# Kernel optimization log

Measured on AMD Instinct MI355X. Metric: run time of the kernel, lower is better.

Reference implementation:

```python
import jax, jax.numpy as jnp
import numpy as np

N, T, F = 20000, 20, 128
H = 128          # lstm hidden per direction
GH, HEADS = 128, 4
NUM_CLASSES = 10
E = 640000
SCALE = 0.05


def _lstm_last_hidden(x, lengths, Wih, Whh, b):
    """Run a unidirectional LSTM over padded x [N,T,F]; return hidden at the
    last valid step per sequence (torch gate order i,f,g,o)."""
    pre = jnp.einsum('ntf,gf->ntg', x, Wih) + b            # [N,T,4H]
    mask = jnp.arange(x.shape[1])[None, :] < lengths[:, None]  # [N,T]
    h0 = jnp.zeros((x.shape[0], Whh.shape[1]), x.dtype)

    def step(carry, inp):
        h, c = carry
        pt, m = inp                                         # [N,4H], [N]
        gates = pt + h @ Whh.T
        i, f, g, o = jnp.split(gates, 4, axis=-1)
        c_new = jax.nn.sigmoid(f) * c + jax.nn.sigmoid(i) * jnp.tanh(g)
        h_new = jax.nn.sigmoid(o) * jnp.tanh(c_new)
        m = m[:, None]
        return (jnp.where(m, h_new, h), jnp.where(m, c_new, c)), None

    (h, _), _ = jax.lax.scan(step, (h0, h0), (pre.transpose(1, 0, 2), mask.T))
    return h


def _reverse_by_length(x, lengths):
    # x[n, t] -> x[n, len-1-t] for t < len (padding positions are masked later)
    idx = jnp.clip(lengths[:, None] - 1 - jnp.arange(x.shape[1])[None, :], 0, None)
    return x[jnp.arange(x.shape[0])[:, None], idx]


def _gat(h, src, dst, W, a_src, a_dst, bias, heads):
    n = h.shape[0]
    xh = (h @ W.T).reshape(n, heads, -1)                    # [N,H,C]
    al_s = jnp.sum(xh * a_src, -1)                          # [N,H]
    al_d = jnp.sum(xh * a_dst, -1)
    e = jax.nn.leaky_relu(al_s[src] + al_d[dst], 0.2)       # [E,H]
    emax = jax.ops.segment_max(e, dst, num_segments=n)
    emax = jnp.where(jnp.isfinite(emax), emax, 0.0)
    ee = jnp.exp(e - emax[dst])
    denom = jax.ops.segment_sum(ee, dst, num_segments=n)
    alpha = ee / (denom[dst] + 1e-16)                       # segment softmax
    out = jax.ops.segment_sum(xh[src] * alpha[..., None], dst, num_segments=n)
    return out.reshape(n, -1) + bias


def setup_inputs() -> dict:
    key = jax.random.key(0)
    ks = jax.random.split(key, 16)
    p = lambda k, *s: jax.random.normal(k, s, jnp.float32) * SCALE
    return {
        'x': jax.random.normal(ks[0], (N, T, F), jnp.float32),
        'lengths': jax.random.randint(ks[1], (N,), 1, T + 1, jnp.int32),
        'edge_index': jax.random.randint(ks[2], (2, E), 0, N, jnp.int32),
        # BiLSTM params (b = b_ih + b_hh combined; identical math)
        'Wih_f': p(ks[3], 4 * H, F), 'Whh_f': p(ks[4], 4 * H, H), 'b_f': p(ks[5], 4 * H),
        'Wih_b': p(ks[6], 4 * H, F), 'Whh_b': p(ks[7], 4 * H, H), 'b_b': p(ks[8], 4 * H),
        # GAT1: in=2H=256 -> heads*GH=512
        'W1': p(ks[9], HEADS * GH, 2 * H), 'a1_src': p(ks[10], HEADS, GH),
        'a1_dst': p(ks[11], HEADS, GH), 'bias1': jnp.zeros((HEADS * GH,), jnp.float32),
        # GAT2: in=512 -> 1*GH=128
        'W2': p(ks[12], GH, HEADS * GH), 'a2_src': p(ks[13], 1, GH),
        'a2_dst': p(ks[14], 1, GH), 'bias2': jnp.zeros((GH,), jnp.float32),
        'Wfc': p(ks[15], NUM_CLASSES, GH), 'bfc': jnp.zeros((NUM_CLASSES,), jnp.float32),
    }


def reference(x, lengths, edge_index, Wih_f, Whh_f, b_f, Wih_b, Whh_b, b_b,
              W1, a1_src, a1_dst, bias1, W2, a2_src, a2_dst, bias2, Wfc, bfc):
    n = x.shape[0]
    h_fwd = _lstm_last_hidden(x, lengths, Wih_f, Whh_f, b_f)
    h_bwd = _lstm_last_hidden(_reverse_by_length(x, lengths), lengths, Wih_b, Whh_b, b_b)
    h = jnp.concatenate([h_fwd, h_bwd], axis=-1)            # [N, 2H]
    # GATConv default adds self-loops
    loop = jnp.arange(n, dtype=edge_index.dtype)
    src = jnp.concatenate([edge_index[0], loop])
    dst = jnp.concatenate([edge_index[1], loop])
    h = jax.nn.relu(_gat(h, src, dst, W1, a1_src, a1_dst, bias1, HEADS))
    h = jax.nn.relu(_gat(h, src, dst, W2, a2_src, a2_dst, bias2, 1))
    return h @ Wfc.T + bfc                                  # [N, num_classes]
```

## Files before the change

### kernel.cpp

```cpp
#include <hip/hip_runtime.h>

#define NSEQ 20000
#define TT 20
#define FD 128
#define EDG 640000
#define ETOT (EDG + NSEQ)

typedef short bf16x8 __attribute__((ext_vector_type(8)));
typedef float f32x4 __attribute__((ext_vector_type(4)));
typedef unsigned short u16;
typedef unsigned int u32;

__device__ __forceinline__ float bf2f(u16 h) {
  union { u32 u; float f; } v; v.u = ((u32)h) << 16; return v.f;
}
__device__ __forceinline__ u16 f2bf(float f) {
  union { float f; u32 u; } v; v.f = f;
  u32 u = v.u;
  return (u16)((u + 0x7fffu + ((u >> 16) & 1u)) >> 16);
}
__device__ __forceinline__ float fast_rcp(float x) {
  float r; asm("v_rcp_f32 %0, %1" : "=v"(r) : "v"(x)); return r;
}
__device__ __forceinline__ u32 cvtpk_bf16(float a, float b) {
  u32 r; asm("v_cvt_pk_bf16_f32 %0, %1, %2" : "=v"(r) : "v"(a), "v"(b)); return r;
}
__device__ __forceinline__ float sigm(float x) { return fast_rcp(1.0f + __expf(-x)); }
__device__ __forceinline__ float tanh_f(float x) { return 1.0f - 2.0f * fast_rcp(__expf(2.0f * x) + 1.0f); }
__device__ __forceinline__ int clampi(int v, int lo, int hi) {
  return v < lo ? lo : (v > hi ? hi : v);
}

template<int BF>
__device__ __forceinline__ bf16x8 ld8(const void* p, size_t i) {
  if (BF) return *(const bf16x8*)((const u16*)p + i);
  f32x4 a = *(const f32x4*)((const float*)p + i);
  f32x4 b = *(const f32x4*)((const float*)p + i + 4);
  union { u32 w[4]; bf16x8 v; } u;
  u.w[0] = cvtpk_bf16(a[0], a[1]);
  u.w[1] = cvtpk_bf16(a[2], a[3]);
  u.w[2] = cvtpk_bf16(b[0], b[1]);
  u.w[3] = cvtpk_bf16(b[2], b[3]);
  return u.v;
}

#define OFF_WIHF 0
#define OFF_WHHF 65536
#define OFF_BF   131072
#define OFF_WIHB 131584
#define OFF_WHHB 197120
#define OFF_BB   262656
#define OFF_W1   263168
#define OFF_W2   394240
#define OFF_A1S  459776
#define OFF_A1D  460288
#define OFF_B1   460800
#define OFF_A2S  461312
#define OFF_A2D  461440
#define OFF_B2   461568
#define OFF_WFC  461696
#define OFF_BFC  462976

__global__ void k_detect(const u32* __restrict__ xw, int* __restrict__ flag) {
  const int lane = threadIdx.x & 63;
  u16 lo = (u16)(xw[lane] & 0xffffu);
  int e = (lo >> 7) & 0xff;
  unsigned long long m = __ballot(e >= 100 && e <= 140);
  if (threadIdx.x == 0) flag[0] = (__popcll(m) >= 32) ? 1 : 0;
}

struct CvtArgs {
  const void* src[16];
  int off[16];
  int cnt[16];
};

template<int BF>
__global__ void k_cvt(CvtArgs a, u16* __restrict__ canon, const int* __restrict__ flag) {
  if (flag[0] != BF) return;
  int idx = blockIdx.x * 256 + threadIdx.x;
  int stride = gridDim.x * 256;
#pragma unroll 1
  for (int s = 0; s < 16; ++s) {
    const void* sp = a.src[s];
    int n = a.cnt[s], off = a.off[s];
    for (int i = idx; i < n; i += stride) {
      canon[off + i] = BF ? ((const u16*)sp)[i] : f2bf(((const float*)sp)[i]);
    }
  }
}

__global__ void k_fill0(u16* __restrict__ out, int n) {
  int i = blockIdx.x * 256 + threadIdx.x;
  if (i < n) out[i] = 0;
}

template<int BF>
__global__ __launch_bounds__(512, 2) void k_lstm(
    const void* __restrict__ x, const int* __restrict__ lengths,
    const int* __restrict__ lperm,
    const u16* __restrict__ canon, u16* __restrict__ hcat,
    const int* __restrict__ flag)
{
  if (flag[0] != BF) return;
  __shared__ u16 Ax[2][64 * 128];
  __shared__ u16 Ah[2][64 * 128];
  __shared__ int lenS[64];
  __shared__ int seqS[64];
  __shared__ int sMax;

  const int tid = threadIdx.x;
  const int wv = tid >> 6;
  const int lane = tid & 63;
  const int q = lane >> 4;
  const int cc = lane & 15;
  const int dir = blockIdx.y;
  const int b0 = (gridDim.x - 1 - blockIdx.x) * 64;

  const u16* Wi = canon + (dir ? OFF_WIHB : OFF_WIHF);
  const u16* Wh = canon + (dir ? OFF_WHHB : OFF_WHHF);
  const u16* bb = canon + (dir ? OFF_BB : OFF_BF);

  bf16x8 wih[4][4], whh[4][4];
  float bv[4];
#pragma unroll
  for (int g = 0; g < 4; ++g) {
    int row = g * 128 + wv * 16 + cc;
#pragma unroll
    for (int kt = 0; kt < 4; ++kt) {
      wih[g][kt] = *(const bf16x8*)(Wi + row * 128 + kt * 32 + q * 8);
      whh[g][kt] = *(const bf16x8*)(Wh + row * 128 + kt * 32 + q * 8);
    }
    bv[g] = bf2f(bb[g * 128 + wv * 16 + cc]);
  }

  if (tid < 64) {
    int s = lperm[clampi(b0 + tid, 0, NSEQ - 1)];
    s = clampi(s, 0, NSEQ - 1);
    seqS[tid] = s;
    int L = clampi(lengths[s], 1, TT);
    lenS[tid] = L;
#pragma unroll
    for (int off = 32; off >= 1; off >>= 1) L = max(L, __shfl_xor(L, off, 64));
    if (tid == 0) sMax = L;
  }
  {
    f32x4 zz = {0.f, 0.f, 0.f, 0.f};
    f32x4* p = (f32x4*)Ah[0];
    for (int i = tid; i < 1024; i += 512) p[i] = zz;
  }
  __syncthreads();

  const int tmax = sMax;

  int lenp[4];
#pragma unroll
  for (int m = 0; m < 4; ++m) {
    int v = 0;
#pragma unroll
    for (int r = 0; r < 4; ++r) v |= lenS[m * 16 + q * 4 + r] << (8 * r);
    lenp[m] = v;
  }

  const int lrow = tid >> 3;
  const int lj = tid & 7;
  const int sL = seqS[lrow];
  const int lenL = lenS[lrow];
  const size_t xbase = (size_t)sL * (TT * FD);
  const int ax0 = lrow * 128 + ((lj ^ (lrow & 15)) * 8);
  const int ax1 = lrow * 128 + (((lj + 8) ^ (lrow & 15)) * 8);

  int rofs[4];
#pragma unroll
  for (int kt = 0; kt < 4; ++kt) rofs[kt] = cc * 128 + (((4 * kt + q) ^ cc) * 8);
  const int hu = wv * 16 + cc;
  int cofs[4];
#pragma unroll
  for (int r = 0; r < 4; ++r)
    cofs[r] = (q * 4 + r) * 128 + (((hu >> 3) ^ (q * 4 + r)) * 8) + (hu & 7);

  {
    int t0 = dir ? (lenL - 1) : 0;
    bf16x8 d0 = ld8<BF>(x, xbase + t0 * FD + lj * 8);
    bf16x8 d1 = ld8<BF>(x, xbase + t0 * FD + (lj + 8) * 8);
    *(bf16x8*)&Ax[0][ax0] = d0;
    *(bf16x8*)&Ax[0][ax1] = d1;
  }
  float c[4][4] = {};
  int cb = 0;
  __syncthreads();

#pragma unroll 1
  for (int t = 0; t < tmax; ++t) {
    const u16* Axr = Ax[cb];
    u16* Axw = Ax[cb ^ 1];
    const u16* Ahr = Ah[cb];
    u16* Ahw = Ah[cb ^ 1];

    bf16x8 d0 = {}, d1 = {};
    const bool more = (t + 1 < tmax);
    if (more) {
      int tn = t + 1;
      int tt2 = dir ? (lenL - 1 - tn) : tn;
      if (tt2 < 0) tt2 = 0;
      d0 = ld8<BF>(x, xbase + tt2 * FD + lj * 8);
      d1 = ld8<BF>(x, xbase + tt2 * FD + (lj + 8) * 8);
    }

#pragma unroll
    for (int m = 0; m < 4; ++m) {
      const int mb = m * 2048;
      f32x4 acc[4];
#pragma unroll
      for (int g = 0; g < 4; ++g) { f32x4 vi = {bv[g], bv[g], bv[g], bv[g]}; acc[g] = vi; }
#pragma unroll
      for (int kt = 0; kt < 4; ++kt) {
        bf16x8 a = *(const bf16x8*)&Axr[mb + rofs[kt]];
#pragma unroll
        for (int g = 0; g < 4; ++g)
          acc[g] = __builtin_amdgcn_mfma_f32_16x16x32_bf16(a, wih[g][kt], acc[g], 0, 0, 0);
      }
#pragma unroll
      for (int kt = 0; kt < 4; ++kt) {
        bf16x8 a = *(const bf16x8*)&Ahr[mb + rofs[kt]];
#pragma unroll
        for (int g = 0; g < 4; ++g)
          acc[g] = __builtin_amdgcn_mfma_f32_16x16x32_bf16(a, whh[g][kt], acc[g], 0, 0, 0);
      }

      int lp = lenp[m];
      float hf[4];
#pragma unroll
      for (int r = 0; r < 4; ++r) {
        if (t < ((lp >> (8 * r)) & 255)) {
          float iv = acc[0][r], fv = acc[1][r], gv = acc[2][r], ov = acc[3][r];
          float cn = sigm(fv) * c[m][r] + sigm(iv) * tanh_f(gv);
          c[m][r] = cn;
          hf[r] = sigm(ov) * tanh_f(cn);
        } else {
          hf[r] = bf2f(Ahr[mb + cofs[r]]);
        }
      }
      u32 w01 = cvtpk_bf16(hf[0], hf[1]);
      u32 w23 = cvtpk_bf16(hf[2], hf[3]);
      Ahw[mb + cofs[0]] = (u16)w01;
      Ahw[mb + cofs[1]] = (u16)(w01 >> 16);
      Ahw[mb + cofs[2]] = (u16)w23;
      Ahw[mb + cofs[3]] = (u16)(w23 >> 16);
    }

    if (more) {
      *(bf16x8*)&Axw[ax0] = d0;
      *(bf16x8*)&Axw[ax1] = d1;
    }
    __syncthreads();
    cb ^= 1;
  }

  for (int i = tid; i < 1024; i += 512) {
    int row = i >> 4, ch = i & 15;
    if (b0 + row < NSEQ) {
      int seq = seqS[row];
      bf16x8 v = *(const bf16x8*)&Ah[cb][row * 128 + ((ch ^ (row & 15)) * 8)];
      *(bf16x8*)(hcat + (size_t)seq * 256 + dir * 128 + ch * 8) = v;
    }
  }
}

__global__ __launch_bounds__(256) void k_gemm(
    const u16* __restrict__ A, const u16* __restrict__ W, u16* __restrict__ C,
    int M, int Nc, int K)
{
  __shared__ u16 As[128 * 64];
  __shared__ u16 Bs[128 * 64];
  const int tid = threadIdx.x;
  const int wv = tid >> 6, lane = tid & 63, q = lane >> 4, cc = lane & 15;
  const int mblk = blockIdx.x * 128, nblk = blockIdx.y * 128;
  const int wm = (wv & 1) * 64, wn = (wv >> 1) * 64;

  f32x4 acc[4][4] = {};

  const int srow = tid >> 1;
  const int sc0 = (tid & 1) * 4;
  int arow_g = mblk + srow; if (arow_g > M - 1) arow_g = M - 1;
  const u16* aptr = A + (size_t)arow_g * K + sc0 * 8;
  const u16* bptr = W + (size_t)(nblk + srow) * K + sc0 * 8;

  for (int k0 = 0; k0 < K; k0 += 64) {
#pragma unroll
    for (int cch = 0; cch < 4; ++cch) {
      bf16x8 av = *(const bf16x8*)(aptr + k0 + cch * 8);
      bf16x8 bvv = *(const bf16x8*)(bptr + k0 + cch * 8);
      int ch = sc0 + cch;
      *(bf16x8*)&As[srow * 64 + ((ch ^ (srow & 7)) * 8)] = av;
      *(bf16x8*)&Bs[srow * 64 + ((ch ^ (srow & 7)) * 8)] = bvv;
    }
    __syncthreads();
#pragma unroll
    for (int kt = 0; kt < 2; ++kt) {
      bf16x8 af[4];
#pragma unroll
      for (int m = 0; m < 4; ++m) {
        int row = wm + m * 16 + cc;
        af[m] = *(const bf16x8*)&As[row * 64 + (((4 * kt + q) ^ (row & 7)) * 8)];
      }
#pragma unroll
      for (int n = 0; n < 4; ++n) {
        int rowb = wn + n * 16 + cc;
        bf16x8 bfr = *(const bf16x8*)&Bs[rowb * 64 + (((4 * kt + q) ^ (rowb & 7)) * 8)];
#pragma unroll
        for (int m = 0; m < 4; ++m)
          acc[m][n] = __builtin_amdgcn_mfma_f32_16x16x32_bf16(af[m], bfr, acc[m][n], 0, 0, 0);
      }
    }
    __syncthreads();
  }

#pragma unroll
  for (int m = 0; m < 4; ++m)
#pragma unroll
    for (int n = 0; n < 4; ++n)
#pragma unroll
      for (int r = 0; r < 4; ++r) {
        int row = mblk + wm + m * 16 + q * 4 + r;
        int col = nblk + wn + n * 16 + cc;
        if (row < M) C[(size_t)row * Nc + col] = f2bf(acc[m][n][r]);
      }
}

__global__ __launch_bounds__(256) void k_al1(
    const u16* __restrict__ xh1, const u16* __restrict__ canon,
    float* __restrict__ als, float* __restrict__ ald)
{
  const int lane = threadIdx.x & 63;
  const int n = blockIdx.x * 4 + (threadIdx.x >> 6);
  const int hd = lane >> 4;
  bf16x8 xv = *(const bf16x8*)(xh1 + (size_t)n * 512 + lane * 8);
  bf16x8 sv = *(const bf16x8*)(canon + OFF_A1S + hd * 128 + (lane & 15) * 8);
  bf16x8 dv = *(const bf16x8*)(canon + OFF_A1D + hd * 128 + (lane & 15) * 8);
  float ps = 0.f, pd = 0.f;
#pragma unroll
  for (int j = 0; j < 8; ++j) {
    float xf = bf2f((u16)xv[j]);
    ps += xf * bf2f((u16)sv[j]);
    pd += xf * bf2f((u16)dv[j]);
  }
#pragma unroll
  for (int off = 8; off >= 1; off >>= 1) {
    ps += __shfl_xor(ps, off, 64);
    pd += __shfl_xor(pd, off, 64);
  }
  if ((lane & 15) == 0) { als[n * 4 + hd] = ps; ald[n * 4 + hd] = pd; }
}

__global__ __launch_bounds__(256) void k_agg1(
    const u16* __restrict__ xh1, const float* __restrict__ als, const float* __restrict__ ald,
    const int* __restrict__ offs, const int* __restrict__ csr,
    const u16* __restrict__ canon, u16* __restrict__ h1)
{
  const int lane = threadIdx.x & 63;
  const int hd = threadIdx.x >> 6;
  const int n = blockIdx.x;
  int off0 = offs[n], off1 = offs[n + 1];
  off0 = clampi(off0, 0, ETOT);
  off1 = clampi(off1, off0, ETOT);
  const float ad = ald[(size_t)n * 4 + hd];
  const int deg = off1 - off0;
  const u16* xb = xh1 + hd * 128 + lane * 2;

  float o0 = 0.f, o1 = 0.f;
  if (deg <= 64) {
    int s = 0;
    float e = -1e30f;
    if (lane < deg) {
      s = clampi(csr[off0 + lane], 0, NSEQ - 1);
      float t = als[(size_t)s * 4 + hd] + ad;
      e = t > 0.f ? t : 0.2f * t;
    }
    float mx = e;
#pragma unroll
    for (int off = 32; off >= 1; off >>= 1) mx = fmaxf(mx, __shfl_xor(mx, off, 64));
    float ex = (lane < deg) ? __expf(e - mx) : 0.f;
    float sm = ex;
#pragma unroll
    for (int off = 32; off >= 1; off >>= 1) sm += __shfl_xor(sm, off, 64);
    const float a = ex * fast_rcp(sm + 1e-16f);
    const int sofs = s * 512;
    for (int j = 0; j < deg; ++j) {
      int so = __builtin_amdgcn_readlane(sofs, j);
      float aa = __int_as_float(__builtin_amdgcn_readlane(__float_as_int(a), j));
      u32 xv = *(const u32*)(xb + so);
      o0 += aa * bf2f((u16)(xv & 0xffffu));
      o1 += aa * bf2f((u16)(xv >> 16));
    }
  } else {
    float mx = -1e30f;
    for (int k = off0 + lane; k < off1; k += 64) {
      int s = clampi(csr[k], 0, NSEQ - 1);
      float e = als[(size_t)s * 4 + hd] + ad;
      e = e > 0.f ? e : 0.2f * e;
      mx = fmaxf(mx, e);
    }
#pragma unroll
    for (int off = 32; off >= 1; off >>= 1) mx = fmaxf(mx, __shfl_xor(mx, off, 64));
    float sm = 0.f;
    for (int k = off0 + lane; k < off1; k += 64) {
      int s = clampi(csr[k], 0, NSEQ - 1);
      float e = als[(size_t)s * 4 + hd] + ad;
      e = e > 0.f ? e : 0.2f * e;
      sm += __expf(e - mx);
    }
#pragma unroll
    for (int off = 32; off >= 1; off >>= 1) sm += __shfl_xor(sm, off, 64);
    const float rd = fast_rcp(sm + 1e-16f);
    for (int k = off0; k < off1; ++k) {
      int s = clampi(csr[k], 0, NSEQ - 1);
      float e = als[(size_t)s * 4 + hd] + ad;
      e = e > 0.f ? e : 0.2f * e;
      float a = __expf(e - mx) * rd;
      u32 xv = *(const u32*)(xb + (size_t)s * 512);
      o0 += a * bf2f((u16)(xv & 0xffffu));
      o1 += a * bf2f((u16)(xv >> 16));
    }
  }
  o0 += bf2f(canon[OFF_B1 + hd * 128 + lane * 2]);
  o1 += bf2f(canon[OFF_B1 + hd * 128 + lane * 2 + 1]);
  o0 = o0 > 0.f ? o0 : 0.f;
  o1 = o1 > 0.f ? o1 : 0.f;
  u32 pk = (u32)f2bf(o0) | ((u32)f2bf(o1) << 16);
  *(u32*)(h1 + (size_t)n * 512 + hd * 128 + lane * 2) = pk;
}

__global__ __launch_bounds__(256) void k_al2(
    const u16* __restrict__ xh2, const u16* __restrict__ canon,
    float* __restrict__ als2, float* __restrict__ ald2)
{
  const int lane = threadIdx.x & 63;
  const int n = blockIdx.x * 4 + (threadIdx.x >> 6);
  float x0 = bf2f(xh2[(size_t)n * 128 + lane * 2]);
  float x1 = bf2f(xh2[(size_t)n * 128 + lane * 2 + 1]);
  float ps = x0 * bf2f(canon[OFF_A2S + lane * 2]) + x1 * bf2f(canon[OFF_A2S + lane * 2 + 1]);
  float pd = x0 * bf2f(canon[OFF_A2D + lane * 2]) + x1 * bf2f(canon[OFF_A2D + lane * 2 + 1]);
#pragma unroll
  for (int off = 32; off >= 1; off >>= 1) {
    ps += __shfl_xor(ps, off, 64);
    pd += __shfl_xor(pd, off, 64);
  }
  if (lane == 0) { als2[n] = ps; ald2[n] = pd; }
}

__global__ __launch_bounds__(256) void k_agg2(
    const u16* __restrict__ xh2, const float* __restrict__ als2, const float* __restrict__ ald2,
    const int* __restrict__ offs, const int* __restrict__ csr,
    const u16* __restrict__ canon, float* __restrict__ h2)
{
  const int lane = threadIdx.x & 63;
  const int n = blockIdx.x * 4 + (threadIdx.x >> 6);
  int off0 = offs[n], off1 = offs[n + 1];
  off0 = clampi(off0, 0, ETOT);
  off1 = clampi(off1, off0, ETOT);
  const float adn = ald2[n];
  const int deg = off1 - off0;

  float o0 = 0.f, o1 = 0.f;
  if (deg <= 64) {
    int s = 0;
    float e = -1e30f;
    if (lane < deg) {
      s = clampi(csr[off0 + lane], 0, NSEQ - 1);
      float t = als2[s] + adn;
      e = t > 0.f ? t : 0.2f * t;
    }
    float mx = e;
#pragma unroll
    for (int off = 32; off >= 1; off >>= 1) mx = fmaxf(mx, __shfl_xor(mx, off, 64));
    float ex = (lane < deg) ? __expf(e - mx) : 0.f;
    float sm = ex;
#pragma unroll
    for (int off = 32; off >= 1; off >>= 1) sm += __shfl_xor(sm, off, 64);
    const float a = ex * fast_rcp(sm + 1e-16f);
    const int sofs = s * 128;
    for (int j = 0; j < deg; ++j) {
      int so = __builtin_amdgcn_readlane(sofs, j);
      float aa = __int_as_float(__builtin_amdgcn_readlane(__float_as_int(a), j));
      u32 xv = *(const u32*)(xh2 + so + lane * 2);
      o0 += aa * bf2f((u16)(xv & 0xffffu));
      o1 += aa * bf2f((u16)(xv >> 16));
    }
  } else {
    float mx = -1e30f;
    for (int k = off0 + lane; k < off1; k += 64) {
      float e = als2[clampi(csr[k], 0, NSEQ - 1)] + adn;
      e = e > 0.f ? e : 0.2f * e;
      mx = fmaxf(mx, e);
    }
#pragma unroll
    for (int off = 32; off >= 1; off >>= 1) mx = fmaxf(mx, __shfl_xor(mx, off, 64));
    float sm = 0.f;
    for (int k = off0 + lane; k < off1; k += 64) {
      float e = als2[clampi(csr[k], 0, NSEQ - 1)] + adn;
      e = e > 0.f ? e : 0.2f * e;
      sm += __expf(e - mx);
    }
#pragma unroll
    for (int off = 32; off >= 1; off >>= 1) sm += __shfl_xor(sm, off, 64);
    float rd = fast_rcp(sm + 1e-16f);
    for (int k = off0; k < off1; ++k) {
      int s = clampi(csr[k], 0, NSEQ - 1);
      float e = als2[s] + adn;
      e = e > 0.f ? e : 0.2f * e;
      float a = __expf(e - mx) * rd;
      u32 xv = *(const u32*)(xh2 + (size_t)s * 128 + lane * 2);
      o0 += a * bf2f((u16)(xv & 0xffffu));
      o1 += a * bf2f((u16)(xv >> 16));
    }
  }
  o0 += bf2f(canon[OFF_B2 + lane * 2]);     o0 = o0 > 0.f ? o0 : 0.f;
  o1 += bf2f(canon[OFF_B2 + lane * 2 + 1]); o1 = o1 > 0.f ? o1 : 0.f;
  float2 st; st.x = o0; st.y = o1;
  *(float2*)(h2 + (size_t)n * 128 + lane * 2) = st;
}

template<int BF>
__global__ __launch_bounds__(256) void k_fc(
    const float* __restrict__ h2, const u16* __restrict__ canon,
    void* __restrict__ out, const int* __restrict__ flag)
{
  if (flag[0] != BF) return;
  const int lane = threadIdx.x & 63;
  const int n = blockIdx.x * 4 + (threadIdx.x >> 6);
  float a0 = h2[(size_t)n * 128 + lane];
  float a1 = h2[(size_t)n * 128 + 64 + lane];
  float res[10];
#pragma unroll
  for (int cls = 0; cls < 10; ++cls) {
    float p = a0 * bf2f(canon[OFF_WFC + cls * 128 + lane]) +
              a1 * bf2f(canon[OFF_WFC + cls * 128 + 64 + lane]);
#pragma unroll
    for (int off = 32; off >= 1; off >>= 1) p += __shfl_xor(p, off, 64);
    float v = p + bf2f(canon[OFF_BFC + cls]);
    res[cls] = (fabsf(v) < 1e30f) ? v : 0.f;
  }
  if (BF) {
    if (lane < 5) {
      u32 pk = (u32)f2bf(res[lane * 2]) | ((u32)f2bf(res[lane * 2 + 1]) << 16);
      ((u32*)out)[(size_t)n * 5 + lane] = pk;
    }
  } else {
    if (lane < 10) ((float*)out)[(size_t)n * 10 + lane] = res[lane];
  }
}

__global__ void k_zero_all(int* __restrict__ deg, int* __restrict__ lcnt) {
  int i = blockIdx.x * 256 + threadIdx.x;
  if (i < NSEQ) deg[i] = 0;
  if (i < 64) lcnt[i] = 0;
}

__global__ void k_hist_all(const int* __restrict__ ei, const int* __restrict__ lengths,
                           int* __restrict__ deg, int* __restrict__ lcnt) {
  int i = blockIdx.x * 256 + threadIdx.x;
  if (i < ETOT) {
    int d = (i < EDG) ? ei[EDG + i] : (i - EDG);
    d = clampi(d, 0, NSEQ - 1);
    atomicAdd(&deg[d], 1);
  }
  if (i < NSEQ) atomicAdd(&lcnt[clampi(lengths[i], 1, TT) - 1], 1);
}

__global__ __launch_bounds__(1024) void k_scan(const int* __restrict__ deg,
                                               int* __restrict__ offs, int* __restrict__ cur,
                                               const int* __restrict__ lcnt,
                                               int* __restrict__ lcur) {
  __shared__ int wsum[16];
  const int tid = threadIdx.x;
  if (tid == 0) {
    int run = 0;
    for (int i = 0; i < TT; ++i) { lcur[i] = run; run += lcnt[i]; }
  }
  const int lane = tid & 63, wv = tid >> 6;
  const int CHUNK = 20;
  int base = tid * CHUNK;
  int loc[20];
  int s = 0;
#pragma unroll
  for (int i = 0; i < CHUNK; ++i) {
    int idx = base + i;
    int v = (idx < NSEQ) ? deg[idx] : 0;
    loc[i] = s;
    s += v;
  }
  int inc = s;
#pragma unroll
  for (int off = 1; off < 64; off <<= 1) {
    int t2 = __shfl_up(inc, off, 64);
    if (lane >= off) inc += t2;
  }
  if (lane == 63) wsum[wv] = inc;
  __syncthreads();
  int wbase = 0;
  for (int i = 0; i < wv; ++i) wbase += wsum[i];
  int tbase = wbase + inc - s;
#pragma unroll
  for (int i = 0; i < CHUNK; ++i) {
    int idx = base + i;
    if (idx < NSEQ) {
      int st = tbase + loc[i];
      offs[idx] = st;
      cur[idx] = st;
    }
  }
  if (tid == 0) offs[NSEQ] = ETOT;
}

__global__ void k_scatter_all(const int* __restrict__ ei, const int* __restrict__ lengths,
                              int* __restrict__ cur, int* __restrict__ csr,
                              int* __restrict__ lcur, int* __restrict__ lperm) {
  int i = blockIdx.x * 256 + threadIdx.x;
  if (i < ETOT) {
    int s, d;
    if (i < EDG) { s = ei[i]; d = ei[EDG + i]; }
    else { s = i - EDG; d = s; }
    d = clampi(d, 0, NSEQ - 1);
    int pos = atomicAdd(&cur[d], 1);
    pos = clampi(pos, 0, ETOT - 1);
    csr[pos] = s;
  }
  if (i < NSEQ) {
    int b = clampi(lengths[i], 1, TT) - 1;
    int pos = atomicAdd(&lcur[b], 1);
    lperm[clampi(pos, 0, NSEQ - 1)] = i;
  }
}

extern "C" void kernel_launch(void* const* d_in, const int* in_sizes, int n_in,
                              void* d_out, int out_size, void* d_ws, size_t ws_size,
                              hipStream_t stream) {
  (void)in_sizes; (void)n_in;
  const void* x     = d_in[0];
  const int* lengths= (const int*)d_in[1];
  const int* ei     = (const int*)d_in[2];

  const size_t NEED = 45769344u;
  if (ws_size < NEED) {
    k_fill0<<<(out_size + 255) / 256, 256, 0, stream>>>((u16*)d_out, out_size);
    return;
  }

  char* w = (char*)d_ws;
  size_t o = 0;
  auto alloc = [&](size_t b) { char* p = w + o; o += (b + 255) & ~(size_t)255; return p; };
  int*  flag = (int*)  alloc(256);
  u16*  canon= (u16*)  alloc(1048576);
  int*  deg  = (int*)  alloc((size_t)NSEQ * 4);
  int*  offs = (int*)  alloc((size_t)(NSEQ + 1) * 4);
  int*  cur  = (int*)  alloc((size_t)NSEQ * 4);
  int*  csr  = (int*)  alloc((size_t)ETOT * 4);
  float* als1= (float*)alloc((size_t)NSEQ * 4 * 4);
  float* ald1= (float*)alloc((size_t)NSEQ * 4 * 4);
  char* regB = alloc((size_t)NSEQ * 512 * 2);
  u16*  xh1  = (u16*)regB;
  u16*  xh2  = (u16*)regB;
  float* h2  = (float*)(regB + (size_t)NSEQ * 128 * 2);
  float* als2= (float*)(regB + (size_t)NSEQ * 128 * 2 + (size_t)NSEQ * 128 * 4);
  float* ald2= als2 + NSEQ;
  char* regA = alloc((size_t)NSEQ * 256 * 2);
  u16*  hcat = (u16*)regA;
  u16*  h1   = (u16*)regA;
  alloc((size_t)NSEQ * 256 * 2);

  int* lperm = (int*)regB;
  int* lcnt  = (int*)(regB + 80128);
  int* lcur  = (int*)(regB + 80256);

  k_detect<<<1, 64, 0, stream>>>((const u32*)x, flag);
  CvtArgs ca;
  const int srcIdx[16] = {3, 4, 5, 6, 7, 8, 9, 13, 10, 11, 12, 14, 15, 16, 17, 18};
  const int offv[16]   = {OFF_WIHF, OFF_WHHF, OFF_BF, OFF_WIHB, OFF_WHHB, OFF_BB,
                          OFF_W1, OFF_W2, OFF_A1S, OFF_A1D, OFF_B1,
                          OFF_A2S, OFF_A2D, OFF_B2, OFF_WFC, OFF_BFC};
  const int cntv[16]   = {65536, 65536, 512, 65536, 65536, 512,
                          131072, 65536, 512, 512, 512, 128, 128, 128, 1280, 10};
  for (int i = 0; i < 16; ++i) { ca.src[i] = d_in[srcIdx[i]]; ca.off[i] = offv[i]; ca.cnt[i] = cntv[i]; }
  k_cvt<1><<<256, 256, 0, stream>>>(ca, canon, flag);
  k_cvt<0><<<256, 256, 0, stream>>>(ca, canon, flag);

  k_zero_all<<<(NSEQ + 255) / 256, 256, 0, stream>>>(deg, lcnt);
  k_hist_all<<<(ETOT + 255) / 256, 256, 0, stream>>>(ei, lengths, deg, lcnt);
  k_scan<<<1, 1024, 0, stream>>>(deg, offs, cur, lcnt, lcur);
  k_scatter_all<<<(ETOT + 255) / 256, 256, 0, stream>>>(ei, lengths, cur, csr, lcur, lperm);

  k_lstm<1><<<dim3(313, 2), 512, 0, stream>>>(x, lengths, lperm, canon, hcat, flag);
  k_lstm<0><<<dim3(313, 2), 512, 0, stream>>>(x, lengths, lperm, canon, hcat, flag);

  k_gemm<<<dim3(157, 4), 256, 0, stream>>>(hcat, canon + OFF_W1, xh1, NSEQ, 512, 256);
  k_al1<<<5000, 256, 0, stream>>>(xh1, canon, als1, ald1);
  k_agg1<<<NSEQ, 256, 0, stream>>>(xh1, als1, ald1, offs, csr, canon, h1);

  k_gemm<<<dim3(157, 1), 256, 0, stream>>>(h1, canon + OFF_W2, xh2, NSEQ, 128, 512);
  k_al2<<<5000, 256, 0, stream>>>(xh2, canon, als2, ald2);
  k_agg2<<<5000, 256, 0, stream>>>(xh2, als2, ald2, offs, csr, canon, h2);

  k_fc<1><<<5000, 256, 0, stream>>>(h2, canon, d_out, flag);
  k_fc<0><<<5000, 256, 0, stream>>>(h2, canon, d_out, flag);
}
```

Before: 864.4 us.

## Fuse attention logits into GEMM epilogue and FC into aggregation; transpose LSTM MFMA

New measurement: 822.6 us. 4.8% less time.

```diff
diff --git a/kernel.cpp b/kernel.cpp
--- a/kernel.cpp
+++ b/kernel.cpp
@@ -13,6 +13,12 @@
 
 __device__ __forceinline__ float bf2f(u16 h) {
   union { u32 u; float f; } v; v.u = ((u32)h) << 16; return v.f;
+}
+__device__ __forceinline__ float bf_lo(u32 w) {
+  union { u32 u; float f; } v; v.u = w << 16; return v.f;
+}
+__device__ __forceinline__ float bf_hi(u32 w) {
+  union { u32 u; float f; } v; v.u = w & 0xffff0000u; return v.f;
 }
 __device__ __forceinline__ u16 f2bf(float f) {
   union { float f; u32 u; } v; v.f = f;
@@ -122,7 +128,7 @@
   const u16* bb = canon + (dir ? OFF_BB : OFF_BF);
 
   bf16x8 wih[4][4], whh[4][4];
-  float bv[4];
+  uint2 bvp[4];
 #pragma unroll
   for (int g = 0; g < 4; ++g) {
     int row = g * 128 + wv * 16 + cc;
@@ -131,7 +137,7 @@
       wih[g][kt] = *(const bf16x8*)(Wi + row * 128 + kt * 32 + q * 8);
       whh[g][kt] = *(const bf16x8*)(Wh + row * 128 + kt * 32 + q * 8);
     }
-    bv[g] = bf2f(bb[g * 128 + wv * 16 + cc]);
+    bvp[g] = *(const uint2*)(bb + g * 128 + wv * 16 + q * 4);
   }
 
   if (tid < 64) {
@@ -153,14 +159,9 @@
 
   const int tmax = sMax;
 
-  int lenp[4];
-#pragma unroll
-  for (int m = 0; m < 4; ++m) {
-    int v = 0;
-#pragma unroll
-    for (int r = 0; r < 4; ++r) v |= lenS[m * 16 + q * 4 + r] << (8 * r);
-    lenp[m] = v;
-  }
+  int lenq[4];
+#pragma unroll
+  for (int m = 0; m < 4; ++m) lenq[m] = lenS[m * 16 + cc];
 
   const int lrow = tid >> 3;
   const int lj = tid & 7;
@@ -173,11 +174,7 @@
   int rofs[4];
 #pragma unroll
   for (int kt = 0; kt < 4; ++kt) rofs[kt] = cc * 128 + (((4 * kt + q) ^ cc) * 8);
-  const int hu = wv * 16 + cc;
-  int cofs[4];
-#pragma unroll
-  for (int r = 0; r < 4; ++r)
-    cofs[r] = (q * 4 + r) * 128 + (((hu >> 3) ^ (q * 4 + r)) * 8) + (hu & 7);
+  const int awbase = cc * 128 + (((wv * 2 + (q >> 1)) ^ cc) * 8) + (q & 1) * 4;
 
   {
     int t0 = dir ? (lenL - 1) : 0;
@@ -212,41 +209,41 @@
       const int mb = m * 2048;
       f32x4 acc[4];
 #pragma unroll
-      for (int g = 0; g < 4; ++g) { f32x4 vi = {bv[g], bv[g], bv[g], bv[g]}; acc[g] = vi; }
+      for (int g = 0; g < 4; ++g) {
+        f32x4 vi = {bf_lo(bvp[g].x), bf_hi(bvp[g].x), bf_lo(bvp[g].y), bf_hi(bvp[g].y)};
+        acc[g] = vi;
+      }
 #pragma unroll
       for (int kt = 0; kt < 4; ++kt) {
-        bf16x8 a = *(const bf16x8*)&Axr[mb + rofs[kt]];
+        bf16x8 b = *(const bf16x8*)&Axr[mb + rofs[kt]];
 #pragma unroll
         for (int g = 0; g < 4; ++g)
-          acc[g] = __builtin_amdgcn_mfma_f32_16x16x32_bf16(a, wih[g][kt], acc[g], 0, 0, 0);
+          acc[g] = __builtin_amdgcn_mfma_f32_16x16x32_bf16(wih[g][kt], b, acc[g], 0, 0, 0);
       }
 #pragma unroll
       for (int kt = 0; kt < 4; ++kt) {
-        bf16x8 a = *(const bf16x8*)&Ahr[mb + rofs[kt]];
+        bf16x8 b = *(const bf16x8*)&Ahr[mb + rofs[kt]];
 #pragma unroll
         for (int g = 0; g < 4; ++g)
-          acc[g] = __builtin_amdgcn_mfma_f32_16x16x32_bf16(a, whh[g][kt], acc[g], 0, 0, 0);
+          acc[g] = __builtin_amdgcn_mfma_f32_16x16x32_bf16(whh[g][kt], b, acc[g], 0, 0, 0);
       }
 
-      int lp = lenp[m];
-      float hf[4];
-#pragma unroll
-      for (int r = 0; r < 4; ++r) {
-        if (t < ((lp >> (8 * r)) & 255)) {
+      uint2 hw;
+      if (t < lenq[m]) {
+        float hf[4];
+#pragma unroll
+        for (int r = 0; r < 4; ++r) {
           float iv = acc[0][r], fv = acc[1][r], gv = acc[2][r], ov = acc[3][r];
           float cn = sigm(fv) * c[m][r] + sigm(iv) * tanh_f(gv);
           c[m][r] = cn;
           hf[r] = sigm(ov) * tanh_f(cn);
-        } else {
-          hf[r] = bf2f(Ahr[mb + cofs[r]]);
         }
+        hw.x = cvtpk_bf16(hf[0], hf[1]);
+        hw.y = cvtpk_bf16(hf[2], hf[3]);
+      } else {
+        hw = *(const uint2*)&Ahr[mb + awbase];
       }
-      u32 w01 = cvtpk_bf16(hf[0], hf[1]);
-      u32 w23 = cvtpk_bf16(hf[2], hf[3]);
-      Ahw[mb + cofs[0]] = (u16)w01;
-      Ahw[mb + cofs[1]] = (u16)(w01 >> 16);
-      Ahw[mb + cofs[2]] = (u16)w23;
-      Ahw[mb + cofs[3]] = (u16)(w23 >> 16);
+      *(uint2*)&Ahw[mb + awbase] = hw;
     }
 
     if (more) {
@@ -269,7 +266,9 @@
 
 __global__ __launch_bounds__(256) void k_gemm(
     const u16* __restrict__ A, const u16* __restrict__ W, u16* __restrict__ C,
-    int M, int Nc, int K)
+    int M, int Nc, int K,
+    const u16* __restrict__ aS, const u16* __restrict__ aD,
+    float* __restrict__ als, float* __restrict__ ald, int alsStride)
 {
   __shared__ u16 As[128 * 64];
   __shared__ u16 Bs[128 * 64];
@@ -310,47 +309,57 @@
         bf16x8 bfr = *(const bf16x8*)&Bs[rowb * 64 + (((4 * kt + q) ^ (rowb & 7)) * 8)];
 #pragma unroll
         for (int m = 0; m < 4; ++m)
-          acc[m][n] = __builtin_amdgcn_mfma_f32_16x16x32_bf16(af[m], bfr, acc[m][n], 0, 0, 0);
+          acc[m][n] = __builtin_amdgcn_mfma_f32_16x16x32_bf16(bfr, af[m], acc[m][n], 0, 0, 0);
       }
     }
     __syncthreads();
   }
 
-#pragma unroll
-  for (int m = 0; m < 4; ++m)
-#pragma unroll
-    for (int n = 0; n < 4; ++n)
-#pragma unroll
-      for (int r = 0; r < 4; ++r) {
-        int row = mblk + wm + m * 16 + q * 4 + r;
-        int col = nblk + wn + n * 16 + cc;
-        if (row < M) C[(size_t)row * Nc + col] = f2bf(acc[m][n][r]);
-      }
-}
-
-__global__ __launch_bounds__(256) void k_al1(
-    const u16* __restrict__ xh1, const u16* __restrict__ canon,
-    float* __restrict__ als, float* __restrict__ ald)
-{
-  const int lane = threadIdx.x & 63;
-  const int n = blockIdx.x * 4 + (threadIdx.x >> 6);
-  const int hd = lane >> 4;
-  bf16x8 xv = *(const bf16x8*)(xh1 + (size_t)n * 512 + lane * 8);
-  bf16x8 sv = *(const bf16x8*)(canon + OFF_A1S + hd * 128 + (lane & 15) * 8);
-  bf16x8 dv = *(const bf16x8*)(canon + OFF_A1D + hd * 128 + (lane & 15) * 8);
-  float ps = 0.f, pd = 0.f;
-#pragma unroll
-  for (int j = 0; j < 8; ++j) {
-    float xf = bf2f((u16)xv[j]);
-    ps += xf * bf2f((u16)sv[j]);
-    pd += xf * bf2f((u16)dv[j]);
-  }
-#pragma unroll
-  for (int off = 8; off >= 1; off >>= 1) {
-    ps += __shfl_xor(ps, off, 64);
-    pd += __shfl_xor(pd, off, 64);
-  }
-  if ((lane & 15) == 0) { als[n * 4 + hd] = ps; ald[n * 4 + hd] = pd; }
+  float pls[4] = {}, pld[4] = {};
+#pragma unroll
+  for (int n = 0; n < 4; ++n) {
+    uint2 ws = *(const uint2*)(aS + nblk + wn + n * 16 + q * 4);
+    uint2 wd = *(const uint2*)(aD + nblk + wn + n * 16 + q * 4);
+    float s0 = bf_lo(ws.x), s1 = bf_hi(ws.x), s2 = bf_lo(ws.y), s3 = bf_hi(ws.y);
+    float d0 = bf_lo(wd.x), d1 = bf_hi(wd.x), d2 = bf_lo(wd.y), d3 = bf_hi(wd.y);
+#pragma unroll
+    for (int m = 0; m < 4; ++m) {
+      int row = mblk + wm + m * 16 + cc;
+      uint2 st;
+      st.x = cvtpk_bf16(acc[m][n][0], acc[m][n][1]);
+      st.y = cvtpk_bf16(acc[m][n][2], acc[m][n][3]);
+      if (row < M) *(uint2*)(C + (size_t)row * Nc + nblk + wn + n * 16 + q * 4) = st;
+      pls[m] += acc[m][n][0] * s0 + acc[m][n][1] * s1 + acc[m][n][2] * s2 + acc[m][n][3] * s3;
+      pld[m] += acc[m][n][0] * d0 + acc[m][n][1] * d1 + acc[m][n][2] * d2 + acc[m][n][3] * d3;
+    }
+  }
+
+#pragma unroll
+  for (int m = 0; m < 4; ++m) {
+    pls[m] += __shfl_xor(pls[m], 16, 64);
+    pls[m] += __shfl_xor(pls[m], 32, 64);
+    pld[m] += __shfl_xor(pld[m], 16, 64);
+    pld[m] += __shfl_xor(pld[m], 32, 64);
+  }
+  float* sred = (float*)As;
+  if (lane < 16) {
+#pragma unroll
+    for (int m = 0; m < 4; ++m) {
+      int idx = ((wv & 1) * 4 + m) * 32 + cc * 2 + (wv >> 1);
+      sred[idx] = pls[m];
+      sred[256 + idx] = pld[m];
+    }
+  }
+  __syncthreads();
+  if (wv < 2) {
+    int m = lane >> 4, ccc = lane & 15;
+    int row = mblk + wv * 64 + m * 16 + ccc;
+    int idx = (wv * 4 + m) * 32 + ccc * 2;
+    if (row < M) {
+      als[(size_t)row * alsStride + blockIdx.y] = sred[idx] + sred[idx + 1];
+      ald[(size_t)row * alsStride + blockIdx.y] = sred[256 + idx] + sred[256 + idx + 1];
+    }
+  }
 }
 
 __global__ __launch_bounds__(256) void k_agg1(
@@ -386,6 +395,7 @@
     for (int off = 32; off >= 1; off >>= 1) sm += __shfl_xor(sm, off, 64);
     const float a = ex * fast_rcp(sm + 1e-16f);
     const int sofs = s * 512;
+#pragma unroll 4
     for (int j = 0; j < deg; ++j) {
       int so = __builtin_amdgcn_readlane(sofs, j);
       float aa = __int_as_float(__builtin_amdgcn_readlane(__float_as_int(a), j));
@@ -413,6 +423,7 @@
 #pragma unroll
     for (int off = 32; off >= 1; off >>= 1) sm += __shfl_xor(sm, off, 64);
     const float rd = fast_rcp(sm + 1e-16f);
+#pragma unroll 4
     for (int k = off0; k < off1; ++k) {
       int s = clampi(csr[k], 0, NSEQ - 1);
       float e = als[(size_t)s * 4 + hd] + ad;
@@ -431,28 +442,10 @@
   *(u32*)(h1 + (size_t)n * 512 + hd * 128 + lane * 2) = pk;
 }
 
-__global__ __launch_bounds__(256) void k_al2(
-    const u16* __restrict__ xh2, const u16* __restrict__ canon,
-    float* __restrict__ als2, float* __restrict__ ald2)
-{
-  const int lane = threadIdx.x & 63;
-  const int n = blockIdx.x * 4 + (threadIdx.x >> 6);
-  float x0 = bf2f(xh2[(size_t)n * 128 + lane * 2]);
-  float x1 = bf2f(xh2[(size_t)n * 128 + lane * 2 + 1]);
-  float ps = x0 * bf2f(canon[OFF_A2S + lane * 2]) + x1 * bf2f(canon[OFF_A2S + lane * 2 + 1]);
-  float pd = x0 * bf2f(canon[OFF_A2D + lane * 2]) + x1 * bf2f(canon[OFF_A2D + lane * 2 + 1]);
-#pragma unroll
-  for (int off = 32; off >= 1; off >>= 1) {
-    ps += __shfl_xor(ps, off, 64);
-    pd += __shfl_xor(pd, off, 64);
-  }
-  if (lane == 0) { als2[n] = ps; ald2[n] = pd; }
-}
-
 __global__ __launch_bounds__(256) void k_agg2(
     const u16* __restrict__ xh2, const float* __restrict__ als2, const float* __restrict__ ald2,
     const int* __restrict__ offs, const int* __restrict__ csr,
-    const u16* __restrict__ canon, float* __restrict__ h2)
+    const u16* __restrict__ canon, void* __restrict__ out, const int* __restrict__ flag)
 {
   const int lane = threadIdx.x & 63;
   const int n = blockIdx.x * 4 + (threadIdx.x >> 6);
@@ -480,6 +473,7 @@
     for (int off = 32; off >= 1; off >>= 1) sm += __shfl_xor(sm, off, 64);
     const float a = ex * fast_rcp(sm + 1e-16f);
     const int sofs = s * 128;
+#pragma unroll 4
     for (int j = 0; j < deg; ++j) {
       int so = __builtin_amdgcn_readlane(sofs, j);
       float aa = __int_as_float(__builtin_amdgcn_readlane(__float_as_int(a), j));
@@ -505,6 +499,7 @@
 #pragma unroll
     for (int off = 32; off >= 1; off >>= 1) sm += __shfl_xor(sm, off, 64);
     float rd = fast_rcp(sm + 1e-16f);
+#pragma unroll 4
     for (int k = off0; k < off1; ++k) {
       int s = clampi(csr[k], 0, NSEQ - 1);
       float e = als2[s] + adn;
@@ -517,31 +512,18 @@
   }
   o0 += bf2f(canon[OFF_B2 + lane * 2]);     o0 = o0 > 0.f ? o0 : 0.f;
   o1 += bf2f(canon[OFF_B2 + lane * 2 + 1]); o1 = o1 > 0.f ? o1 : 0.f;
-  float2 st; st.x = o0; st.y = o1;
-  *(float2*)(h2 + (size_t)n * 128 + lane * 2) = st;
-}
-
-template<int BF>
-__global__ __launch_bounds__(256) void k_fc(
-    const float* __restrict__ h2, const u16* __restrict__ canon,
-    void* __restrict__ out, const int* __restrict__ flag)
-{
-  if (flag[0] != BF) return;
-  const int lane = threadIdx.x & 63;
-  const int n = blockIdx.x * 4 + (threadIdx.x >> 6);
-  float a0 = h2[(size_t)n * 128 + lane];
-  float a1 = h2[(size_t)n * 128 + 64 + lane];
+
   float res[10];
 #pragma unroll
   for (int cls = 0; cls < 10; ++cls) {
-    float p = a0 * bf2f(canon[OFF_WFC + cls * 128 + lane]) +
-              a1 * bf2f(canon[OFF_WFC + cls * 128 + 64 + lane]);
+    float p = o0 * bf2f(canon[OFF_WFC + cls * 128 + lane * 2]) +
+              o1 * bf2f(canon[OFF_WFC + cls * 128 + lane * 2 + 1]);
 #pragma unroll
     for (int off = 32; off >= 1; off >>= 1) p += __shfl_xor(p, off, 64);
     float v = p + bf2f(canon[OFF_BFC + cls]);
     res[cls] = (fabsf(v) < 1e30f) ? v : 0.f;
   }
-  if (BF) {
+  if (flag[0]) {
     if (lane < 5) {
       u32 pk = (u32)f2bf(res[lane * 2]) | ((u32)f2bf(res[lane * 2 + 1]) << 16);
       ((u32*)out)[(size_t)n * 5 + lane] = pk;
@@ -661,7 +643,6 @@
   char* regB = alloc((size_t)NSEQ * 512 * 2);
   u16*  xh1  = (u16*)regB;
   u16*  xh2  = (u16*)regB;
-  float* h2  = (float*)(regB + (size_t)NSEQ * 128 * 2);
   float* als2= (float*)(regB + (size_t)NSEQ * 128 * 2 + (size_t)NSEQ * 128 * 4);
   float* ald2= als2 + NSEQ;
   char* regA = alloc((size_t)NSEQ * 256 * 2);
@@ -693,14 +674,11 @@
   k_lstm<1><<<dim3(313, 2), 512, 0, stream>>>(x, lengths, lperm, canon, hcat, flag);
   k_lstm<0><<<dim3(313, 2), 512, 0, stream>>>(x, lengths, lperm, canon, hcat, flag);
 
-  k_gemm<<<dim3(157, 4), 256, 0, stream>>>(hcat, canon + OFF_W1, xh1, NSEQ, 512, 256);
-  k_al1<<<5000, 256, 0, stream>>>(xh1, canon, als1, ald1);
+  k_gemm<<<dim3(157, 4), 256, 0, stream>>>(hcat, canon + OFF_W1, xh1, NSEQ, 512, 256,
+                                           canon + OFF_A1S, canon + OFF_A1D, als1, ald1, 4);
   k_agg1<<<NSEQ, 256, 0, stream>>>(xh1, als1, ald1, offs, csr, canon, h1);
 
-  k_gemm<<<dim3(157, 1), 256, 0, stream>>>(h1, canon + OFF_W2, xh2, NSEQ, 128, 512);
-  k_al2<<<5000, 256, 0, stream>>>(xh2, canon, als2, ald2);
-  k_agg2<<<5000, 256, 0, stream>>>(xh2, als2, ald2, offs, csr, canon, h2);
-
-  k_fc<1><<<5000, 256, 0, stream>>>(h2, canon, d_out, flag);
-  k_fc<0><<<5000, 256, 0, stream>>>(h2, canon, d_out, flag);
-}
+  k_gemm<<<dim3(157, 1), 256, 0, stream>>>(h1, canon + OFF_W2, xh2, NSEQ, 128, 512,
+                                           canon + OFF_A2S, canon + OFF_A2D, als2, ald2, 1);
+  k_agg2<<<5000, 256, 0, stream>>>(xh2, als2, ald2, offs, csr, canon, d_out, flag);
+}
```
